# Performance work log

Measured on AMD Instinct MI355X. Metric: run time of the kernel, lower is better.

Reference implementation:

```python
import jax, jax.numpy as jnp
import numpy as np

N, H = 100000, 64
ARITIES = (1, 2, 3)
COUNTS = (500000, 800000, 600000)  # flattened index lengths (multiple of arity)


def _mlp(x, w1, b1, w2, b2):
    return jnp.maximum(x @ w1 + b1, 0.0) @ w2 + b2


def setup_inputs() -> dict:
    key = jax.random.key(0)
    ks = jax.random.split(key, 16)
    inp = {"node_states": jax.random.normal(ks[0], (N, H), jnp.float32)}
    for r, c in enumerate(COUNTS):
        inp[f"rel{r}_idx"] = jax.random.randint(ks[1 + r], (c,), 0, N, jnp.int32)
    ki = 4
    for r, a in enumerate(ARITIES):
        d = a * H
        inp[f"r{r}_w1"] = jax.random.normal(ks[ki], (d, d), jnp.float32) * 0.02; ki += 1
        inp[f"r{r}_b1"] = jnp.zeros((d,), jnp.float32)
        inp[f"r{r}_w2"] = jax.random.normal(ks[ki], (d, d), jnp.float32) * 0.02; ki += 1
        inp[f"r{r}_b2"] = jnp.zeros((d,), jnp.float32)
    inp["up_w1"] = jax.random.normal(ks[ki], (2 * H, 2 * H), jnp.float32) * 0.02; ki += 1
    inp["up_b1"] = jnp.zeros((2 * H,), jnp.float32)
    inp["up_w2"] = jax.random.normal(ks[ki], (2 * H, H), jnp.float32) * 0.02
    inp["up_b2"] = jnp.zeros((H,), jnp.float32)
    return inp


def reference(node_states, rel0_idx, rel1_idx, rel2_idx,
              r0_w1, r0_b1, r0_w2, r0_b2,
              r1_w1, r1_b1, r1_w2, r1_b2,
              r2_w1, r2_b1, r2_w2, r2_b2,
              up_w1, up_b1, up_w2, up_b2):
    rels = [(rel0_idx, ARITIES[0], (r0_w1, r0_b1, r0_w2, r0_b2)),
            (rel1_idx, ARITIES[1], (r1_w1, r1_b1, r1_w2, r1_b2)),
            (rel2_idx, ARITIES[2], (r2_w1, r2_b1, r2_w2, r2_b2))]
    outs = []
    for idx, a, p in rels:
        # gather node features, group tuples of `a` nodes, per-relation MLP
        x = node_states[idx].reshape(-1, a * H)         # [E_r, a*H]
        out = _mlp(x, *p).reshape(-1, H)                # [E_r*a, H]: one message per participant node
        outs.append((out, idx))
    max_offset = jnp.max(jnp.stack([o.max() for o, _ in outs]))
    exps_sum = jnp.full((node_states.shape[0], H), 1e-16, node_states.dtype)
    for out, idx in outs:
        exps_sum = exps_sum + jax.ops.segment_sum(
            jnp.exp(8.0 * (out - max_offset)), idx, num_segments=node_states.shape[0])
    max_msg = jnp.log(exps_sum) / 8.0 + max_offset     # smooth-max aggregation
    return _mlp(jnp.concatenate([max_msg, node_states], axis=1), up_w1, up_b1, up_w2, up_b2)
```

## Files before the change

kernel.cpp:

```cpp
#include <hip/hip_runtime.h>
#include <hip/hip_fp16.h>
#include <math.h>


typedef __attribute__((ext_vector_type(8))) short bf16x8;
typedef __attribute__((ext_vector_type(4))) float f32x4;
typedef __attribute__((ext_vector_type(8))) _Float16 f16x8;
typedef unsigned short u16;

__device__ __forceinline__ u16 f2bf(float f) {
    unsigned u = __float_as_uint(f);
    return (u16)((u + 0x7fffu + ((u >> 16) & 1u)) >> 16);
}

__global__ __launch_bounds__(256) void conv_states(const float* __restrict__ src,
                                                   u16* __restrict__ dst, int n8) {
    int i = blockIdx.x * 256 + threadIdx.x;
    if (i >= n8) return;
    float4 a = reinterpret_cast<const float4*>(src)[2 * i];
    float4 b = reinterpret_cast<const float4*>(src)[2 * i + 1];
    bf16x8 v;
    v[0] = (short)f2bf(a.x); v[1] = (short)f2bf(a.y);
    v[2] = (short)f2bf(a.z); v[3] = (short)f2bf(a.w);
    v[4] = (short)f2bf(b.x); v[5] = (short)f2bf(b.y);
    v[6] = (short)f2bf(b.z); v[7] = (short)f2bf(b.w);
    reinterpret_cast<bf16x8*>(dst)[i] = v;
}

struct TEnt { const float* src; u16* dst; int K, N, base; float scale; };
struct TPack { TEnt e[8]; };
__global__ __launch_bounds__(256) void transpose_w(TPack p) {
    int b = blockIdx.x;
    int i = 0;
    while (i < 7 && b >= p.e[i + 1].base) ++i;
    TEnt e = p.e[i];
    int idx = (b - e.base) * 256 + threadIdx.x;
    if (idx < e.K * e.N) {
        int n = idx / e.K, k = idx - n * e.K;
        e.dst[idx] = f2bf(e.scale * e.src[k * e.N + n]);
    }
}

__global__ __launch_bounds__(256) void hist_k(const int* __restrict__ idx, int n,
                                              int* __restrict__ hist) {
    int i = blockIdx.x * 256 + threadIdx.x;
    if (i < n) atomicAdd(&hist[idx[i]], 1);
}

template <int D>
__device__ __forceinline__ void rel_body(
    const u16* __restrict__ statesb, const int* __restrict__ idx,
    const u16* __restrict__ W1t, const float* __restrict__ B1,
    const u16* __restrict__ W2t, const float* __restrict__ B2,
    __half* __restrict__ exps, float* __restrict__ bmslot, int E, int bid,
    u16* Xs, int* Ids, float* wmax) {
    constexpr int A = D / 64;
    constexpr int KF = D / 32;
    constexpr int NFW = D / 64;
    constexpr int CPR = D / 8;
    char* Xc = (char*)Xs;

    const int tid = threadIdx.x;
    const int block0 = bid * 64;
    const int validRows = min(64, E - block0);
    const int validSegs = validRows * A;
    const long long segBase = (long long)block0 * A;

    for (int q = tid; q < 64 * CPR; q += 256) {
        int r = q / CPR, c = q - r * CPR;
        int slot = c >> 3;
        int wc = (c & 7) ^ (r & 7);
        int seg = r * A + slot;
        bf16x8 v = {};
        if (seg < validSegs) {
            int node = idx[segBase + seg];
            v = *reinterpret_cast<const bf16x8*>(statesb + (long long)node * 64 + wc * 8);
            if ((c & 7) == 0) Ids[seg] = node;
        }
        *reinterpret_cast<bf16x8*>(Xc + q * 16) = v;
    }
    __syncthreads();

    const int l = tid & 63;
    const int ln = l & 15, kq = l >> 4;
    const int w = tid >> 6;
    const int nbase = w * NFW;

    f32x4 acc[4][NFW];

    #pragma unroll
    for (int nf = 0; nf < NFW; ++nf) {
        float b = B1[(nbase + nf) * 16 + ln];
        #pragma unroll
        for (int m = 0; m < 4; ++m) acc[m][nf] = {b, b, b, b};
    }
    #pragma unroll
    for (int kf = 0; kf < KF; ++kf) {
        bf16x8 a[4];
        #pragma unroll
        for (int m = 0; m < 4; ++m)
            a[m] = *reinterpret_cast<const bf16x8*>(
                Xc + (m * 16 + ln) * (2 * D) + ((kf * 64 + kq * 16) ^ ((ln & 7) << 4)));
        #pragma unroll
        for (int nf = 0; nf < NFW; ++nf) {
            bf16x8 b = *reinterpret_cast<const bf16x8*>(
                W1t + ((nbase + nf) * 16 + ln) * D + kf * 32 + kq * 8);
            #pragma unroll
            for (int m = 0; m < 4; ++m)
                acc[m][nf] = __builtin_amdgcn_mfma_f32_16x16x32_bf16(a[m], b, acc[m][nf], 0, 0, 0);
        }
    }
    __syncthreads();
    #pragma unroll
    for (int nf = 0; nf < NFW; ++nf) {
        const int c = (nbase + nf) * 16 + ln;
        #pragma unroll
        for (int m = 0; m < 4; ++m)
            #pragma unroll
            for (int j = 0; j < 4; ++j) {
                int row = m * 16 + kq * 4 + j;
                int byte = (c * 2) ^ ((row & 7) << 4);
                *reinterpret_cast<u16*>(Xc + row * (2 * D) + byte) =
                    f2bf(fmaxf(acc[m][nf][j], 0.f));
            }
    }
    __syncthreads();

    #pragma unroll
    for (int nf = 0; nf < NFW; ++nf) {
        float b = 8.f * B2[(nbase + nf) * 16 + ln];
        #pragma unroll
        for (int m = 0; m < 4; ++m) acc[m][nf] = {b, b, b, b};
    }
    #pragma unroll
    for (int kf = 0; kf < KF; ++kf) {
        bf16x8 a[4];
        #pragma unroll
        for (int m = 0; m < 4; ++m)
            a[m] = *reinterpret_cast<const bf16x8*>(
                Xc + (m * 16 + ln) * (2 * D) + ((kf * 64 + kq * 16) ^ ((ln & 7) << 4)));
        #pragma unroll
        for (int nf = 0; nf < NFW; ++nf) {
            bf16x8 b = *reinterpret_cast<const bf16x8*>(
                W2t + ((nbase + nf) * 16 + ln) * D + kf * 32 + kq * 8);
            #pragma unroll
            for (int m = 0; m < 4; ++m)
                acc[m][nf] = __builtin_amdgcn_mfma_f32_16x16x32_bf16(a[m], b, acc[m][nf], 0, 0, 0);
        }
    }

    float m = -INFINITY;
    #pragma unroll
    for (int mf = 0; mf < 4; ++mf)
        #pragma unroll
        for (int nf = 0; nf < NFW; ++nf)
            #pragma unroll
            for (int j = 0; j < 4; ++j) {
                int row = mf * 16 + kq * 4 + j;
                if (row < validRows) m = fmaxf(m, acc[mf][nf][j]);
            }
    #pragma unroll
    for (int off = 32; off; off >>= 1) m = fmaxf(m, __shfl_xor(m, off));
    if (l == 0) wmax[w] = m;
    __syncthreads();
    if (tid == 0)
        *bmslot = 0.125f * fmaxf(fmaxf(wmax[0], wmax[1]), fmaxf(wmax[2], wmax[3]));

    _Float16* Xh = (_Float16*)Xc;
    #pragma unroll
    for (int nf = 0; nf < NFW; ++nf) {
        const int c = (nbase + nf) * 16 + ln;
        const int slot = c >> 6;
        const int feat = c & 63;
        #pragma unroll
        for (int mf = 0; mf < 4; ++mf)
            #pragma unroll
            for (int j = 0; j < 4; ++j) {
                int row = mf * 16 + kq * 4 + j;
                Xh[(row * A + slot) * 64 + feat] = (_Float16)__expf(acc[mf][nf][j]);
            }
    }
    __syncthreads();

    {
        constexpr int SPW = 16 * A;
        const int fp = l & 31;
        for (int s0 = w * SPW; s0 < (w + 1) * SPW; s0 += 2) {
            int seg = s0 + (l >> 5);
            if (seg < validSegs) {
                int node = Ids[seg];
                __half2 pk = *reinterpret_cast<const __half2*>(Xc + seg * 128 + fp * 4);
                unsafeAtomicAdd(reinterpret_cast<__half2*>(
                    exps + (long long)node * 64 + fp * 2), pk);
            }
        }
    }
}

__device__ __forceinline__ void rel0_body(
    const u16* __restrict__ statesb, const int* __restrict__ cnt,
    const u16* __restrict__ W1t, const float* __restrict__ B1,
    const u16* __restrict__ W2t, const float* __restrict__ B2,
    __half* __restrict__ exps, float* __restrict__ bmslot, int Nn, int bid,
    u16* Xs, float* wmax) {
    constexpr int D = 64, KF = 2, CPR = 8;
    char* Xc = (char*)Xs;
    const int tid = threadIdx.x;
    const int block0 = bid * 64;
    const int validRows = min(64, Nn - block0);

    for (int q = tid; q < 64 * CPR; q += 256) {
        int r = q / CPR, c = q - r * CPR;
        int wc = (c & 7) ^ (r & 7);
        bf16x8 v = {};
        if (r < validRows)
            v = *reinterpret_cast<const bf16x8*>(
                statesb + (long long)(block0 + r) * 64 + wc * 8);
        *reinterpret_cast<bf16x8*>(Xc + q * 16) = v;
    }
    __syncthreads();

    const int l = tid & 63;
    const int ln = l & 15, kq = l >> 4;
    const int w = tid >> 6;

    f32x4 acc[4];
    {
        float b = B1[w * 16 + ln];
        #pragma unroll
        for (int m = 0; m < 4; ++m) acc[m] = {b, b, b, b};
    }
    #pragma unroll
    for (int kf = 0; kf < KF; ++kf) {
        bf16x8 a[4];
        #pragma unroll
        for (int m = 0; m < 4; ++m)
            a[m] = *reinterpret_cast<const bf16x8*>(
                Xc + (m * 16 + ln) * (2 * D) + ((kf * 64 + kq * 16) ^ ((ln & 7) << 4)));
        bf16x8 b = *reinterpret_cast<const bf16x8*>(
            W1t + (w * 16 + ln) * D + kf * 32 + kq * 8);
        #pragma unroll
        for (int m = 0; m < 4; ++m)
            acc[m] = __builtin_amdgcn_mfma_f32_16x16x32_bf16(a[m], b, acc[m], 0, 0, 0);
    }
    __syncthreads();
    #pragma unroll
    for (int m = 0; m < 4; ++m)
        #pragma unroll
        for (int j = 0; j < 4; ++j) {
            int row = m * 16 + kq * 4 + j;
            int byte = ((w * 16 + ln) * 2) ^ ((row & 7) << 4);
            *reinterpret_cast<u16*>(Xc + row * (2 * D) + byte) =
                f2bf(fmaxf(acc[m][j], 0.f));
        }
    __syncthreads();
    {
        float b = 8.f * B2[w * 16 + ln];
        #pragma unroll
        for (int m = 0; m < 4; ++m) acc[m] = {b, b, b, b};
    }
    #pragma unroll
    for (int kf = 0; kf < KF; ++kf) {
        bf16x8 a[4];
        #pragma unroll
        for (int m = 0; m < 4; ++m)
            a[m] = *reinterpret_cast<const bf16x8*>(
                Xc + (m * 16 + ln) * (2 * D) + ((kf * 64 + kq * 16) ^ ((ln & 7) << 4)));
        bf16x8 b = *reinterpret_cast<const bf16x8*>(
            W2t + (w * 16 + ln) * D + kf * 32 + kq * 8);
        #pragma unroll
        for (int m = 0; m < 4; ++m)
            acc[m] = __builtin_amdgcn_mfma_f32_16x16x32_bf16(a[m], b, acc[m], 0, 0, 0);
    }

    float m = -INFINITY;
    int cn[4][4];
    #pragma unroll
    for (int mf = 0; mf < 4; ++mf)
        #pragma unroll
        for (int j = 0; j < 4; ++j) {
            int row = mf * 16 + kq * 4 + j;
            cn[mf][j] = (row < validRows) ? cnt[block0 + row] : 0;
            if (cn[mf][j] > 0) m = fmaxf(m, acc[mf][j]);
        }
    #pragma unroll
    for (int off = 32; off; off >>= 1) m = fmaxf(m, __shfl_xor(m, off));
    if (l == 0) wmax[w] = m;
    __syncthreads();
    if (tid == 0)
        *bmslot = 0.125f * fmaxf(fmaxf(wmax[0], wmax[1]), fmaxf(wmax[2], wmax[3]));

    _Float16* Xh = (_Float16*)Xc;
    const int feat = w * 16 + ln;
    #pragma unroll
    for (int mf = 0; mf < 4; ++mf)
        #pragma unroll
        for (int j = 0; j < 4; ++j) {
            int row = mf * 16 + kq * 4 + j;
            Xh[row * 64 + feat] = (_Float16)((float)cn[mf][j] * __expf(acc[mf][j]));
        }
    __syncthreads();

    {
        const int fp = l & 31;
        for (int s0 = w * 16; s0 < (w + 1) * 16; s0 += 2) {
            int row = s0 + (l >> 5);
            if (row < validRows && cnt[block0 + row] > 0) {
                __half2 pk = *reinterpret_cast<const __half2*>(Xc + row * 128 + fp * 4);
                unsafeAtomicAdd(reinterpret_cast<__half2*>(
                    exps + (long long)(block0 + row) * 64 + fp * 2), pk);
            }
        }
    }
}

struct RelArgs {
    const u16* statesb;
    const int* cnt0; const int* idx1; const int* idx2;
    const u16* w1t0; const float* b10; const u16* w2t0; const float* b20;
    const u16* w1t1; const float* b11; const u16* w2t1; const float* b21;
    const u16* w1t2; const float* b12; const u16* w2t2; const float* b22;
    __half* exps;
    float* blockmax;
    int Nn, E1, E2, G0, G01;
};

__global__ __launch_bounds__(256) void rel_fused(RelArgs a) {
    __shared__ __align__(16) u16 Xs[64 * 192];
    __shared__ int Ids[64 * 3];
    __shared__ float wmax[4];
    const int bid = blockIdx.x;
    if (bid < a.G0)
        rel0_body(a.statesb, a.cnt0, a.w1t0, a.b10, a.w2t0, a.b20,
                  a.exps, a.blockmax + bid, a.Nn, bid, Xs, wmax);
    else if (bid < a.G01)
        rel_body<128>(a.statesb, a.idx1, a.w1t1, a.b11, a.w2t1, a.b21,
                      a.exps, a.blockmax + bid, a.E1, bid - a.G0, Xs, Ids, wmax);
    else
        rel_body<192>(a.statesb, a.idx2, a.w1t2, a.b12, a.w2t2, a.b22,
                      a.exps, a.blockmax + bid, a.E2, bid - a.G01, Xs, Ids, wmax);
}

__global__ __launch_bounds__(256) void reduce_max(const float* __restrict__ bm,
                                                  int n, float* __restrict__ out) {
    __shared__ float ws_[4];
    float m = -INFINITY;
    for (int i = threadIdx.x; i < n; i += 256) m = fmaxf(m, bm[i]);
    #pragma unroll
    for (int off = 32; off; off >>= 1) m = fmaxf(m, __shfl_xor(m, off));
    if ((threadIdx.x & 63) == 0) ws_[threadIdx.x >> 6] = m;
    __syncthreads();
    if (threadIdx.x == 0)
        out[0] = fmaxf(fmaxf(ws_[0], ws_[1]), fmaxf(ws_[2], ws_[3]));
}

__global__ __launch_bounds__(256) void up_mfma(
    const u16* __restrict__ statesb, const _Float16* __restrict__ exps,
    const float* __restrict__ gmaxp,
    const u16* __restrict__ W1t, const float* __restrict__ B1,
    const u16* __restrict__ W2t, const float* __restrict__ B2,
    float* __restrict__ outp, int Nn) {
    constexpr int D = 128;
    __shared__ __align__(16) u16 Xs[64 * D];
    char* Xc = (char*)Xs;
    const int tid = threadIdx.x;
    const int block0 = blockIdx.x * 64;
    const int validRows = min(64, Nn - block0);
    const float M = gmaxp[0];
    const float EM = __expf(-8.f * M);

    for (int q = tid; q < 64 * 16; q += 256) {
        int r = q >> 4, p = q & 15;
        bf16x8 v = {};
        if (r < validRows) {
            long long nd = block0 + r;
            if (p < 8) {
                f16x8 s = *reinterpret_cast<const f16x8*>(exps + nd * 64 + p * 8);
                #pragma unroll
                for (int i = 0; i < 8; ++i)
                    v[i] = (short)f2bf(__logf(1e-16f + (float)s[i] * EM) * 0.125f + M);
            } else {
                v = *reinterpret_cast<const bf16x8*>(statesb + nd * 64 + (p - 8) * 8);
            }
        }
        int byte = (p * 16) ^ ((r & 7) << 4);
        *reinterpret_cast<bf16x8*>(Xc + r * 256 + byte) = v;
    }
    __syncthreads();

    const int l = tid & 63;
    const int ln = l & 15, kq = l >> 4;
    const int row0 = (tid >> 6) * 16;

    f32x4 acc[8];
    #pragma unroll
    for (int n = 0; n < 8; ++n) {
        float b = B1[n * 16 + ln];
        acc[n] = {b, b, b, b};
    }
    {
        const u16* wb = W1t + ln * D + kq * 8;
        #pragma unroll
        for (int kf = 0; kf < 4; ++kf) {
            bf16x8 a = *reinterpret_cast<const bf16x8*>(
                Xc + (row0 + ln) * 256 + ((kf * 64 + kq * 16) ^ ((ln & 7) << 4)));
            #pragma unroll
            for (int n = 0; n < 8; ++n) {
                bf16x8 b = *reinterpret_cast<const bf16x8*>(wb + n * 16 * D + kf * 32);
                acc[n] = __builtin_amdgcn_mfma_f32_16x16x32_bf16(a, b, acc[n], 0, 0, 0);
            }
        }
    }
    #pragma unroll
    for (int n = 0; n < 8; ++n) {
        #pragma unroll
        for (int j = 0; j < 4; ++j) {
            int rl = kq * 4 + j;
            int byte = ((n * 16 + ln) * 2) ^ ((rl & 7) << 4);
            *reinterpret_cast<u16*>(Xc + (row0 + rl) * 256 + byte) =
                f2bf(fmaxf(acc[n][j], 0.f));
        }
    }
    f32x4 acc2[4];
    #pragma unroll
    for (int n = 0; n < 4; ++n) {
        float b = B2[n * 16 + ln];
        acc2[n] = {b, b, b, b};
    }
    {
        const u16* wb = W2t + ln * D + kq * 8;
        #pragma unroll
        for (int kf = 0; kf < 4; ++kf) {
            bf16x8 a = *reinterpret_cast<const bf16x8*>(
                Xc + (row0 + ln) * 256 + ((kf * 64 + kq * 16) ^ ((ln & 7) << 4)));
            #pragma unroll
            for (int n = 0; n < 4; ++n) {
                bf16x8 b = *reinterpret_cast<const bf16x8*>(wb + n * 16 * D + kf * 32);
                acc2[n] = __builtin_amdgcn_mfma_f32_16x16x32_bf16(a, b, acc2[n], 0, 0, 0);
            }
        }
    }
    #pragma unroll
    for (int n = 0; n < 4; ++n)
        #pragma unroll
        for (int j = 0; j < 4; ++j) {
            int row = row0 + kq * 4 + j;
            if (row < validRows)
                outp[(long long)(block0 + row) * 64 + n * 16 + ln] = acc2[n][j];
        }
}

extern "C" void kernel_launch(void* const* d_in, const int* in_sizes, int n_in,
                              void* d_out, int out_size, void* d_ws, size_t ws_size,
                              hipStream_t stream) {
    const float* states = (const float*)d_in[0];
    const int* idxp[3] = {(const int*)d_in[1], (const int*)d_in[2], (const int*)d_in[3]};
    const float* rw1[3] = {(const float*)d_in[4], (const float*)d_in[8], (const float*)d_in[12]};
    const float* rb1[3] = {(const float*)d_in[5], (const float*)d_in[9], (const float*)d_in[13]};
    const float* rw2[3] = {(const float*)d_in[6], (const float*)d_in[10], (const float*)d_in[14]};
    const float* rb2[3] = {(const float*)d_in[7], (const float*)d_in[11], (const float*)d_in[15]};
    const float* upw1 = (const float*)d_in[16];
    const float* upb1 = (const float*)d_in[17];
    const float* upw2 = (const float*)d_in[18];
    const float* upb2 = (const float*)d_in[19];

    const int N = in_sizes[0] / 64;
    const int L0 = in_sizes[1];
    const int E1 = in_sizes[2] / 2;
    const int E2 = in_sizes[3] / 3;
    const int G0 = (N + 63) / 64;
    const int G1 = (E1 + 63) / 64, G2 = (E2 + 63) / 64;
    const int Gtot = G0 + G1 + G2;
    const int Dd[3] = {64, 128, 192};

    size_t off = 0;
    auto alloc = [&](size_t bytes) {
        void* p = (char*)d_ws + off;
        off += (bytes + 255) & ~(size_t)255;
        return p;
    };
    float* gmaxf = (float*)alloc(4);
    float* blockmax = (float*)alloc((size_t)Gtot * 4);
    __half* exps = (__half*)alloc((size_t)N * 64 * 2);
    int* hist0 = (int*)alloc((size_t)N * 4);
    size_t zlen = (size_t)((char*)hist0 - (char*)exps) + (size_t)N * 4;
    u16* statesb = (u16*)alloc((size_t)N * 64 * 2);
    u16* w1t[3], *w2t[3];
    for (int r = 0; r < 3; ++r) {
        w1t[r] = (u16*)alloc((size_t)Dd[r] * Dd[r] * 2);
        w2t[r] = (u16*)alloc((size_t)Dd[r] * Dd[r] * 2);
    }
    u16* upw1t = (u16*)alloc(128 * 128 * 2);
    u16* upw2t = (u16*)alloc(64 * 128 * 2);

    (void)hipMemsetAsync(exps, 0, zlen, stream);

    conv_states<<<dim3((N * 64 / 8 + 255) / 256), dim3(256), 0, stream>>>(
        states, statesb, N * 64 / 8);

    TPack tp;
    const float* tsrc[8] = {rw1[0], rw2[0], rw1[1], rw2[1], rw1[2], rw2[2], upw1, upw2};
    u16* tdst[8] = {w1t[0], w2t[0], w1t[1], w2t[1], w1t[2], w2t[2], upw1t, upw2t};
    const int tK[8] = {64, 64, 128, 128, 192, 192, 128, 128};
    const int tN[8] = {64, 64, 128, 128, 192, 192, 128, 64};
    const float tsc[8] = {1.f, 8.f, 1.f, 8.f, 1.f, 8.f, 1.f, 1.f};
    int base = 0;
    for (int i = 0; i < 8; ++i) {
        tp.e[i] = {tsrc[i], tdst[i], tK[i], tN[i], base, tsc[i]};
        base += (tK[i] * tN[i] + 255) / 256;
    }
    transpose_w<<<dim3(base), dim3(256), 0, stream>>>(tp);

    hist_k<<<dim3((L0 + 255) / 256), dim3(256), 0, stream>>>(idxp[0], L0, hist0);

    RelArgs ra;
    ra.statesb = statesb;
    ra.cnt0 = hist0; ra.idx1 = idxp[1]; ra.idx2 = idxp[2];
    ra.w1t0 = w1t[0]; ra.b10 = rb1[0]; ra.w2t0 = w2t[0]; ra.b20 = rb2[0];
    ra.w1t1 = w1t[1]; ra.b11 = rb1[1]; ra.w2t1 = w2t[1]; ra.b21 = rb2[1];
    ra.w1t2 = w1t[2]; ra.b12 = rb1[2]; ra.w2t2 = w2t[2]; ra.b22 = rb2[2];
    ra.exps = exps;
    ra.blockmax = blockmax;
    ra.Nn = N; ra.E1 = E1; ra.E2 = E2; ra.G0 = G0; ra.G01 = G0 + G1;

    rel_fused<<<dim3(Gtot), dim3(256), 0, stream>>>(ra);

    reduce_max<<<dim3(1), dim3(256), 0, stream>>>(blockmax, Gtot, gmaxf);

    up_mfma<<<dim3((N + 63) / 64), dim3(256), 0, stream>>>(
        statesb, (const _Float16*)exps, gmaxf, upw1t, upb1, upw2t, upb2,
        (float*)d_out, N);
}
```

Before: 345.1 us.

## Replace half2 atomic scatter with CSR bucketing and per-node reduction

The fp16 atomic scatter of messages into the exps accumulator is replaced by a CSR scheme. Histogram kernels count messages per node for relations 1 and 2, and a three-pass scan builds node offsets and cursors. The fused relation kernel then writes each message into a slot claimed from the per-node cursor, while relation 0 writes a dense per-node buffer. A separate reduce kernel sums each node's contiguous messages in fp32 and writes exps. This removes contention on the feature-wide half2 atomics, but it adds a large message buffer with an extra write and read pass, several small launches, and one cursor atomic per segment. The old atomic path remains as a fallback when the workspace is too small.

```diff
diff --git a/kernel.cpp b/kernel.cpp
--- a/kernel.cpp
+++ b/kernel.cpp
@@ -47,12 +47,77 @@
     if (i < n) atomicAdd(&hist[idx[i]], 1);
 }
 
-template <int D>
+__global__ __launch_bounds__(256) void scanA(const int* __restrict__ hist, int N,
+                                             int* __restrict__ partial) {
+    __shared__ int ts[256];
+    int b = blockIdx.x, t = threadIdx.x;
+    int i0 = b * 1024 + t * 4;
+    int s = 0;
+    #pragma unroll
+    for (int q = 0; q < 4; ++q) s += (i0 + q < N) ? hist[i0 + q] : 0;
+    ts[t] = s;
+    __syncthreads();
+    for (int off = 128; off; off >>= 1) {
+        if (t < off) ts[t] += ts[t + off];
+        __syncthreads();
+    }
+    if (t == 0) partial[b] = ts[0];
+}
+
+__global__ __launch_bounds__(256) void scanB(int* __restrict__ partial, int B1) {
+    __shared__ int ts[256];
+    int t = threadIdx.x;
+    int v = (t < B1) ? partial[t] : 0;
+    ts[t] = v;
+    __syncthreads();
+    for (int off = 1; off < 256; off <<= 1) {
+        int x = (t >= off) ? ts[t - off] : 0;
+        __syncthreads();
+        ts[t] += x;
+        __syncthreads();
+    }
+    if (t < B1) partial[t] = ts[t] - v;
+}
+
+__global__ __launch_bounds__(256) void scanC(const int* __restrict__ hist, int N,
+                                             const int* __restrict__ partial,
+                                             int* __restrict__ nodeStart,
+                                             int* __restrict__ cursor) {
+    __shared__ int ts[256];
+    int b = blockIdx.x, t = threadIdx.x;
+    int i0 = b * 1024 + t * 4;
+    int v[4];
+    int s = 0;
+    #pragma unroll
+    for (int q = 0; q < 4; ++q) { v[q] = (i0 + q < N) ? hist[i0 + q] : 0; s += v[q]; }
+    ts[t] = s;
+    __syncthreads();
+    for (int off = 1; off < 256; off <<= 1) {
+        int x = (t >= off) ? ts[t - off] : 0;
+        __syncthreads();
+        ts[t] += x;
+        __syncthreads();
+    }
+    int run = partial[b] + ts[t] - s;
+    #pragma unroll
+    for (int q = 0; q < 4; ++q) {
+        int i = i0 + q;
+        if (i < N) {
+            nodeStart[i] = run;
+            cursor[i] = run;
+            if (i == N - 1) nodeStart[N] = run + v[q];
+            run += v[q];
+        }
+    }
+}
+
+template <int D, int MODE>
 __device__ __forceinline__ void rel_body(
     const u16* __restrict__ statesb, const int* __restrict__ idx,
     const u16* __restrict__ W1t, const float* __restrict__ B1,
     const u16* __restrict__ W2t, const float* __restrict__ B2,
-    __half* __restrict__ exps, float* __restrict__ bmslot, int E, int bid,
+    __half* __restrict__ exps, int* __restrict__ cursor,
+    _Float16* __restrict__ msgbuf, float* __restrict__ bmslot, int E, int bid,
     u16* Xs, int* Ids, float* wmax) {
     constexpr int A = D / 64;
     constexpr int KF = D / 32;
@@ -87,7 +152,6 @@
     const int nbase = w * NFW;
 
     f32x4 acc[4][NFW];
-
     #pragma unroll
     for (int nf = 0; nf < NFW; ++nf) {
         float b = B1[(nbase + nf) * 16 + ln];
@@ -187,22 +251,35 @@
         const int fp = l & 31;
         for (int s0 = w * SPW; s0 < (w + 1) * SPW; s0 += 2) {
             int seg = s0 + (l >> 5);
-            if (seg < validSegs) {
-                int node = Ids[seg];
-                __half2 pk = *reinterpret_cast<const __half2*>(Xc + seg * 128 + fp * 4);
-                unsafeAtomicAdd(reinterpret_cast<__half2*>(
-                    exps + (long long)node * 64 + fp * 2), pk);
-            }
-        }
-    }
-}
-
+            if (MODE == 0) {
+                if (seg < validSegs) {
+                    int node = Ids[seg];
+                    __half2 pk = *reinterpret_cast<const __half2*>(Xc + seg * 128 + fp * 4);
+                    unsafeAtomicAdd(reinterpret_cast<__half2*>(
+                        exps + (long long)node * 64 + fp * 2), pk);
+                }
+            } else {
+                int pos = 0;
+                if (seg < validSegs && (l & 31) == 0)
+                    pos = atomicAdd(&cursor[Ids[seg]], 1);
+                pos = __shfl(pos, l & 32);
+                if (seg < validSegs) {
+                    __half2 pk = *reinterpret_cast<const __half2*>(Xc + seg * 128 + fp * 4);
+                    *reinterpret_cast<__half2*>((__half*)msgbuf +
+                        (long long)pos * 64 + fp * 2) = pk;
+                }
+            }
+        }
+    }
+}
+
+template <int MODE>
 __device__ __forceinline__ void rel0_body(
     const u16* __restrict__ statesb, const int* __restrict__ cnt,
     const u16* __restrict__ W1t, const float* __restrict__ B1,
     const u16* __restrict__ W2t, const float* __restrict__ B2,
-    __half* __restrict__ exps, float* __restrict__ bmslot, int Nn, int bid,
-    u16* Xs, float* wmax) {
+    __half* __restrict__ exps, _Float16* __restrict__ r0v,
+    float* __restrict__ bmslot, int Nn, int bid, u16* Xs, float* wmax) {
     constexpr int D = 64, KF = 2, CPR = 8;
     char* Xc = (char*)Xs;
     const int tid = threadIdx.x;
@@ -305,10 +382,15 @@
         const int fp = l & 31;
         for (int s0 = w * 16; s0 < (w + 1) * 16; s0 += 2) {
             int row = s0 + (l >> 5);
-            if (row < validRows && cnt[block0 + row] > 0) {
-                __half2 pk = *reinterpret_cast<const __half2*>(Xc + row * 128 + fp * 4);
-                unsafeAtomicAdd(reinterpret_cast<__half2*>(
-                    exps + (long long)(block0 + row) * 64 + fp * 2), pk);
+            if (row >= validRows) continue;
+            __half2 pk = *reinterpret_cast<const __half2*>(Xc + row * 128 + fp * 4);
+            if (MODE == 0) {
+                if (cnt[block0 + row] > 0)
+                    unsafeAtomicAdd(reinterpret_cast<__half2*>(
+                        exps + (long long)(block0 + row) * 64 + fp * 2), pk);
+            } else {
+                *reinterpret_cast<__half2*>((__half*)r0v +
+                    (long long)(block0 + row) * 64 + fp * 2) = pk;
             }
         }
     }
@@ -321,24 +403,43 @@
     const u16* w1t1; const float* b11; const u16* w2t1; const float* b21;
     const u16* w1t2; const float* b12; const u16* w2t2; const float* b22;
     __half* exps;
+    int* cursor;
+    _Float16* msgbuf;
+    _Float16* r0v;
     float* blockmax;
     int Nn, E1, E2, G0, G01;
 };
 
+template <int MODE>
 __global__ __launch_bounds__(256) void rel_fused(RelArgs a) {
     __shared__ __align__(16) u16 Xs[64 * 192];
     __shared__ int Ids[64 * 3];
     __shared__ float wmax[4];
     const int bid = blockIdx.x;
     if (bid < a.G0)
-        rel0_body(a.statesb, a.cnt0, a.w1t0, a.b10, a.w2t0, a.b20,
-                  a.exps, a.blockmax + bid, a.Nn, bid, Xs, wmax);
+        rel0_body<MODE>(a.statesb, a.cnt0, a.w1t0, a.b10, a.w2t0, a.b20,
+                        a.exps, a.r0v, a.blockmax + bid, a.Nn, bid, Xs, wmax);
     else if (bid < a.G01)
-        rel_body<128>(a.statesb, a.idx1, a.w1t1, a.b11, a.w2t1, a.b21,
-                      a.exps, a.blockmax + bid, a.E1, bid - a.G0, Xs, Ids, wmax);
+        rel_body<128, MODE>(a.statesb, a.idx1, a.w1t1, a.b11, a.w2t1, a.b21,
+                            a.exps, a.cursor, a.msgbuf, a.blockmax + bid,
+                            a.E1, bid - a.G0, Xs, Ids, wmax);
     else
-        rel_body<192>(a.statesb, a.idx2, a.w1t2, a.b12, a.w2t2, a.b22,
-                      a.exps, a.blockmax + bid, a.E2, bid - a.G01, Xs, Ids, wmax);
+        rel_body<192, MODE>(a.statesb, a.idx2, a.w1t2, a.b12, a.w2t2, a.b22,
+                            a.exps, a.cursor, a.msgbuf, a.blockmax + bid,
+                            a.E2, bid - a.G01, Xs, Ids, wmax);
+}
+
+__global__ __launch_bounds__(256) void reduce_k(const _Float16* __restrict__ msgbuf,
+                                                const int* __restrict__ nodeStart,
+                                                const _Float16* __restrict__ r0v,
+                                                __half* __restrict__ exps, int Nn) {
+    int node = (blockIdx.x * 256 + threadIdx.x) >> 6;
+    if (node >= Nn) return;
+    int lane = threadIdx.x & 63;
+    int s = nodeStart[node], e = nodeStart[node + 1];
+    float S = (float)r0v[(long long)node * 64 + lane];
+    for (int i = s; i < e; ++i) S += (float)msgbuf[(long long)i * 64 + lane];
+    exps[(long long)node * 64 + lane] = __float2half(S);
 }
 
 __global__ __launch_bounds__(256) void reduce_max(const float* __restrict__ bm,
@@ -465,13 +566,14 @@
     const float* upb2 = (const float*)d_in[19];
 
     const int N = in_sizes[0] / 64;
-    const int L0 = in_sizes[1];
-    const int E1 = in_sizes[2] / 2;
-    const int E2 = in_sizes[3] / 3;
+    const int L0 = in_sizes[1], L1 = in_sizes[2], L2 = in_sizes[3];
+    const int E1 = L1 / 2, E2 = L2 / 3;
+    const long long P12 = (long long)L1 + L2;
     const int G0 = (N + 63) / 64;
     const int G1 = (E1 + 63) / 64, G2 = (E2 + 63) / 64;
     const int Gtot = G0 + G1 + G2;
     const int Dd[3] = {64, 128, 192};
+    const int B1n = (N + 1023) / 1024;
 
     size_t off = 0;
     auto alloc = [&](size_t bytes) {
@@ -482,8 +584,12 @@
     float* gmaxf = (float*)alloc(4);
     float* blockmax = (float*)alloc((size_t)Gtot * 4);
     __half* exps = (__half*)alloc((size_t)N * 64 * 2);
-    int* hist0 = (int*)alloc((size_t)N * 4);
-    size_t zlen = (size_t)((char*)hist0 - (char*)exps) + (size_t)N * 4;
+    int* cnt0 = (int*)alloc((size_t)N * 4);
+    int* hist12 = (int*)alloc((size_t)N * 4);
+    int* nodeStart = (int*)alloc((size_t)(N + 1) * 4);
+    int* partial = (int*)alloc(4096);
+    int* cursor = (int*)alloc((size_t)N * 4);
+    _Float16* r0v = (_Float16*)alloc((size_t)N * 64 * 2);
     u16* statesb = (u16*)alloc((size_t)N * 64 * 2);
     u16* w1t[3], *w2t[3];
     for (int r = 0; r < 3; ++r) {
@@ -492,8 +598,8 @@
     }
     u16* upw1t = (u16*)alloc(128 * 128 * 2);
     u16* upw2t = (u16*)alloc(64 * 128 * 2);
-
-    (void)hipMemsetAsync(exps, 0, zlen, stream);
+    _Float16* msgbuf = (_Float16*)alloc((size_t)P12 * 64 * 2);
+    const bool csr = (off <= ws_size);
 
     conv_states<<<dim3((N * 64 / 8 + 255) / 256), dim3(256), 0, stream>>>(
         states, statesb, N * 64 / 8);
@@ -511,19 +617,39 @@
     }
     transpose_w<<<dim3(base), dim3(256), 0, stream>>>(tp);
 
-    hist_k<<<dim3((L0 + 255) / 256), dim3(256), 0, stream>>>(idxp[0], L0, hist0);
-
     RelArgs ra;
     ra.statesb = statesb;
-    ra.cnt0 = hist0; ra.idx1 = idxp[1]; ra.idx2 = idxp[2];
+    ra.cnt0 = cnt0; ra.idx1 = idxp[1]; ra.idx2 = idxp[2];
     ra.w1t0 = w1t[0]; ra.b10 = rb1[0]; ra.w2t0 = w2t[0]; ra.b20 = rb2[0];
     ra.w1t1 = w1t[1]; ra.b11 = rb1[1]; ra.w2t1 = w2t[1]; ra.b21 = rb2[1];
     ra.w1t2 = w1t[2]; ra.b12 = rb1[2]; ra.w2t2 = w2t[2]; ra.b22 = rb2[2];
     ra.exps = exps;
+    ra.cursor = cursor;
+    ra.msgbuf = msgbuf;
+    ra.r0v = r0v;
     ra.blockmax = blockmax;
     ra.Nn = N; ra.E1 = E1; ra.E2 = E2; ra.G0 = G0; ra.G01 = G0 + G1;
 
-    rel_fused<<<dim3(Gtot), dim3(256), 0, stream>>>(ra);
+    if (csr) {
+        size_t zoff = (char*)cnt0 - (char*)d_ws;
+        size_t zlen = ((char*)hist12 - (char*)cnt0) + (size_t)N * 4;
+        (void)hipMemsetAsync((char*)d_ws + zoff, 0, zlen, stream);
+        hist_k<<<dim3((L0 + 255) / 256), dim3(256), 0, stream>>>(idxp[0], L0, cnt0);
+        hist_k<<<dim3((L1 + 255) / 256), dim3(256), 0, stream>>>(idxp[1], L1, hist12);
+        hist_k<<<dim3((L2 + 255) / 256), dim3(256), 0, stream>>>(idxp[2], L2, hist12);
+        scanA<<<dim3(B1n), dim3(256), 0, stream>>>(hist12, N, partial);
+        scanB<<<dim3(1), dim3(256), 0, stream>>>(partial, B1n);
+        scanC<<<dim3(B1n), dim3(256), 0, stream>>>(hist12, N, partial, nodeStart, cursor);
+        rel_fused<1><<<dim3(Gtot), dim3(256), 0, stream>>>(ra);
+        reduce_k<<<dim3(((size_t)N * 64 + 255) / 256), dim3(256), 0, stream>>>(
+            msgbuf, nodeStart, r0v, exps, N);
+    } else {
+        size_t zoff = (char*)exps - (char*)d_ws;
+        size_t zlen = ((char*)cnt0 - (char*)exps) + (size_t)N * 4;
+        (void)hipMemsetAsync((char*)d_ws + zoff, 0, zlen, stream);
+        hist_k<<<dim3((L0 + 255) / 256), dim3(256), 0, stream>>>(idxp[0], L0, cnt0);
+        rel_fused<0><<<dim3(Gtot), dim3(256), 0, stream>>>(ra);
+    }
 
     reduce_max<<<dim3(1), dim3(256), 0, stream>>>(blockmax, Gtot, gmaxf);
 
```

Measured after the change: 511.9 us. 48.3% more time.
